# Kernel tuning notes

Measured on AMD Instinct MI355X. Metric: run time of the kernel, lower is better.

Reference implementation:

```python
import jax, jax.numpy as jnp
import numpy as np


def setup_inputs() -> dict:
    key = jax.random.key(0)
    kq, kk, kv = jax.random.split(key, 3)
    B, N, M, H, D = 4, 2048, 2048, 8, 64
    queries = jax.random.normal(kq, (B, N, H, D), dtype=jnp.float32)
    keys = jax.random.normal(kk, (B, M, H, D), dtype=jnp.float32)
    values = jax.random.normal(kv, (B, M, H, D), dtype=jnp.float32)
    return {"queries": queries, "keys": keys, "values": values}


def reference(queries, keys, values):
    # queries: [B,N,H,D], keys/values: [B,M,H,D]
    D = queries.shape[3]
    softmax_temp = 1.0 / (D ** 0.5)
    QK = jnp.einsum('bnhd,bmhd->bnmh', queries, keys)  # [B,N,M,H]
    A = jax.nn.softmax(softmax_temp * QK, axis=2)      # softmax over M
    queried_values = jnp.einsum('bnmh,bmhd->bnhd', A, values)
    attention_weight = jnp.transpose(A, (0, 3, 1, 2))  # [B,H,N,M]
    return (queried_values, attention_weight)
```

## Files before the change

kernel.cpp:

```cpp
#include <hip/hip_runtime.h>

typedef __bf16 bf16x8 __attribute__((ext_vector_type(8)));
typedef float floatx4 __attribute__((ext_vector_type(4)));
typedef unsigned short ushort8 __attribute__((ext_vector_type(8)));
typedef unsigned short ushort4v __attribute__((ext_vector_type(4)));

#define MFMA(a, b, c) __builtin_amdgcn_mfma_f32_16x16x32_bf16((a), (b), (c), 0, 0, 0)

__device__ __forceinline__ unsigned short f2bf(float x) {
  union { float f; unsigned u; } v; v.f = x;
  unsigned r = v.u + 0x7FFFu + ((v.u >> 16) & 1u);
  return (unsigned short)(r >> 16);
}

__global__ __launch_bounds__(256)
void prep(const float* __restrict__ K, const float* __restrict__ V,
          unsigned short* __restrict__ Kb, unsigned short* __restrict__ Vt)
{
  int id = blockIdx.x * 256 + threadIdx.x;
  int isV = id >> 19;
  int cch = id & 524287;
  int bh = cch >> 14;
  int mt = (cch >> 9) & 31;
  int g  = cch & 511;
  int r  = g >> 3;
  int s  = g & 7;
  int e8 = s ^ (r & 7);
  int b = bh >> 3, h = bh & 7;
  ushort8 o;
  if (!isV) {
    const float* p = K + (((size_t)(b * 2048 + mt * 64 + r) * 8 + h) * 64 + e8 * 8);
    float4 x0 = *(const float4*)p;
    float4 x1 = *(const float4*)(p + 4);
    o[0] = f2bf(x0.x); o[1] = f2bf(x0.y); o[2] = f2bf(x0.z); o[3] = f2bf(x0.w);
    o[4] = f2bf(x1.x); o[5] = f2bf(x1.y); o[6] = f2bf(x1.z); o[7] = f2bf(x1.w);
    *(ushort8*)(Kb + (size_t)cch * 8) = o;
  } else {
    const float* p = V + (((size_t)(b * 2048 + mt * 64 + e8 * 8) * 8 + h) * 64 + r);
    #pragma unroll
    for (int j = 0; j < 8; ++j) o[j] = f2bf(p[(size_t)j * 512]);
    *(ushort8*)(Vt + (size_t)cch * 8) = o;
  }
}

__device__ __forceinline__ void stage2k(const unsigned short* gsrc, unsigned short* lds,
                                        int w, int l)
{
  const char* g = (const char*)gsrc + w * 2048 + l * 16;
  char* sd = (char*)lds + w * 2048;
  __builtin_amdgcn_global_load_lds((const __attribute__((address_space(1))) unsigned int*)g,
                                   (__attribute__((address_space(3))) unsigned int*)sd, 16, 0, 0);
  __builtin_amdgcn_global_load_lds((const __attribute__((address_space(1))) unsigned int*)(g + 1024),
                                   (__attribute__((address_space(3))) unsigned int*)(sd + 1024), 16, 0, 0);
}

__device__ __forceinline__ bf16x8 frag(const unsigned short* lds, int r, int bo)
{
  int slot = ((bo >> 4) ^ r) & 7;
  return *(const bf16x8*)((const char*)lds + r * 128 + (slot << 4));
}

__global__ __launch_bounds__(256, 4)
void attn_fwd(const float* __restrict__ Q, const unsigned short* __restrict__ Kb,
              const unsigned short* __restrict__ Vt,
              float* __restrict__ outQV, float* __restrict__ outA)
{
  __shared__ __align__(16) unsigned short Ks[2][4096];
  __shared__ __align__(16) unsigned short Vs[2][4096];
  __shared__ __align__(16) unsigned short As[4096];

  const int tid = threadIdx.x;
  const int w  = tid >> 6;
  const int l  = tid & 63;
  const int c  = l & 15;
  const int q4 = l >> 4;

  const int bx = (blockIdx.x & 7) * 128 + (blockIdx.x >> 3);
  const int qt = bx & 31;
  const int h  = (bx >> 5) & 7;
  const int b  = bx >> 8;
  const int q0 = qt * 64;

  const float scale = 0.125f * 1.44269504088896340736f;

  const size_t base = (size_t)b * (2048 * 512) + (size_t)h * 64;
  const float* Qb = Q + base + (size_t)q0 * 512;

  const unsigned short* Kt0 = Kb + (size_t)(b * 8 + h) * (32 * 4096);
  const unsigned short* Vt0 = Vt + (size_t)(b * 8 + h) * (32 * 4096);

  bf16x8 bQ0, bQ1;
  {
    const float* qp = Qb + (size_t)(16 * w + c) * 512 + q4 * 8;
    float4 qa0 = *(const float4*)(qp);
    float4 qa1 = *(const float4*)(qp + 4);
    float4 qb0 = *(const float4*)(qp + 32);
    float4 qb1 = *(const float4*)(qp + 36);
    ushort8 t0, t1;
    t0[0]=f2bf(qa0.x*scale); t0[1]=f2bf(qa0.y*scale); t0[2]=f2bf(qa0.z*scale); t0[3]=f2bf(qa0.w*scale);
    t0[4]=f2bf(qa1.x*scale); t0[5]=f2bf(qa1.y*scale); t0[6]=f2bf(qa1.z*scale); t0[7]=f2bf(qa1.w*scale);
    t1[0]=f2bf(qb0.x*scale); t1[1]=f2bf(qb0.y*scale); t1[2]=f2bf(qb0.z*scale); t1[3]=f2bf(qb0.w*scale);
    t1[4]=f2bf(qb1.x*scale); t1[5]=f2bf(qb1.y*scale); t1[6]=f2bf(qb1.z*scale); t1[7]=f2bf(qb1.w*scale);
    bQ0 = __builtin_bit_cast(bf16x8, t0);
    bQ1 = __builtin_bit_cast(bf16x8, t1);
  }

  stage2k(Kt0, Ks[0], w, l);
  float lsum[4] = {0.f, 0.f, 0.f, 0.f};
  int cur = 0;
  for (int mt = 0; mt < 32; ++mt) {
    __syncthreads();
    if (mt + 1 < 32) stage2k(Kt0 + (size_t)(mt + 1) * 4096, Ks[cur ^ 1], w, l);
    const unsigned short* Kc = Ks[cur];
    __builtin_amdgcn_s_setprio(1);
    #pragma unroll
    for (int t = 0; t < 4; ++t) {
      bf16x8 aK0 = frag(Kc, t * 16 + c, q4 * 16);
      bf16x8 aK1 = frag(Kc, t * 16 + c, 64 + q4 * 16);
      floatx4 acc = {0.f, 0.f, 0.f, 0.f};
      acc = MFMA(aK0, bQ0, acc);
      acc = MFMA(aK1, bQ1, acc);
      #pragma unroll
      for (int i = 0; i < 4; ++i) lsum[i] += __builtin_amdgcn_exp2f(acc[i]);
    }
    __builtin_amdgcn_s_setprio(0);
    cur ^= 1;
  }
  float rs = (lsum[0] + lsum[1]) + (lsum[2] + lsum[3]);
  rs += __shfl_xor(rs, 16);
  rs += __shfl_xor(rs, 32);
  const float rcp = 1.0f / rs;

  floatx4 Oacc[4];
  #pragma unroll
  for (int t = 0; t < 4; ++t) Oacc[t] = (floatx4){0.f, 0.f, 0.f, 0.f};

  const int arow = 16 * w + c;
  float* aRowP = outA + (((size_t)(b * 8 + h) * 2048 + q0 + arow) * 2048) + q4 * 4;

  __syncthreads();
  stage2k(Kt0, Ks[0], w, l);
  stage2k(Vt0, Vs[0], w, l);
  asm volatile("s_waitcnt vmcnt(0)" ::: "memory");
  __builtin_amdgcn_s_barrier();
  __builtin_amdgcn_sched_barrier(0);
  cur = 0;
  for (int mt = 0; mt < 32; ++mt) {
    if (mt + 1 < 32) {
      stage2k(Kt0 + (size_t)(mt + 1) * 4096, Ks[cur ^ 1], w, l);
      stage2k(Vt0 + (size_t)(mt + 1) * 4096, Vs[cur ^ 1], w, l);
    }
    const unsigned short* Kc = Ks[cur];
    const unsigned short* Vc = Vs[cur];
    const int mc = mt * 64;
    __builtin_amdgcn_s_setprio(1);
    #pragma unroll
    for (int t = 0; t < 4; ++t) {
      bf16x8 aK0 = frag(Kc, t * 16 + c, q4 * 16);
      bf16x8 aK1 = frag(Kc, t * 16 + c, 64 + q4 * 16);
      floatx4 acc = {0.f, 0.f, 0.f, 0.f};
      acc = MFMA(aK0, bQ0, acc);
      acc = MFMA(aK1, bQ1, acc);
      floatx4 av;
      av[0] = __builtin_amdgcn_exp2f(acc[0]) * rcp;
      av[1] = __builtin_amdgcn_exp2f(acc[1]) * rcp;
      av[2] = __builtin_amdgcn_exp2f(acc[2]) * rcp;
      av[3] = __builtin_amdgcn_exp2f(acc[3]) * rcp;
      *(floatx4*)(aRowP + mc + t * 16) = av;
      ushort4v us = { f2bf(av[0]), f2bf(av[1]), f2bf(av[2]), f2bf(av[3]) };
      int bo = t * 32 + q4 * 8;
      int slot = ((bo >> 4) ^ arow) & 7;
      *(ushort4v*)((char*)As + arow * 128 + (slot << 4) + (bo & 15)) = us;
    }
    bf16x8 aP0 = frag(As, arow, q4 * 16);
    bf16x8 aP1 = frag(As, arow, 64 + q4 * 16);
    #pragma unroll
    for (int t = 0; t < 4; ++t) {
      bf16x8 bV0 = frag(Vc, t * 16 + c, q4 * 16);
      bf16x8 bV1 = frag(Vc, t * 16 + c, 64 + q4 * 16);
      Oacc[t] = MFMA(aP0, bV0, Oacc[t]);
      Oacc[t] = MFMA(aP1, bV1, Oacc[t]);
    }
    __builtin_amdgcn_s_setprio(0);
    __builtin_amdgcn_sched_barrier(0);
    asm volatile("s_waitcnt vmcnt(4)" ::: "memory");
    __builtin_amdgcn_s_barrier();
    __builtin_amdgcn_sched_barrier(0);
    cur ^= 1;
  }

  #pragma unroll
  for (int t = 0; t < 4; ++t) {
    #pragma unroll
    for (int i = 0; i < 4; ++i) {
      outQV[base + (size_t)(q0 + 16 * w + q4 * 4 + i) * 512 + t * 16 + c] = Oacc[t][i];
    }
  }
}

extern "C" void kernel_launch(void* const* d_in, const int* in_sizes, int n_in,
                              void* d_out, int out_size, void* d_ws, size_t ws_size,
                              hipStream_t stream)
{
  const float* Q = (const float*)d_in[0];
  const float* K = (const float*)d_in[1];
  const float* V = (const float*)d_in[2];
  float* outQV = (float*)d_out;
  float* outA  = (float*)d_out + 4194304;

  unsigned short* Kb = (unsigned short*)d_ws;
  unsigned short* Vt = (unsigned short*)d_ws + 4194304;

  prep<<<dim3(4096), dim3(256), 0, stream>>>(K, V, Kb, Vt);
  attn_fwd<<<dim3(1024), dim3(256), 0, stream>>>(Q, Kb, Vt, outQV, outA);
}
```

Measured before the change: 634.0 us.

## Double query tile per block and triple-buffer K/V with prefetch distance two

Each block now has 8 waves and covers 128 query rows instead of 64, so every K/V tile staged into LDS serves twice as many queries. Global-to-LDS traffic and block count are halved. K and V staging becomes a three-buffer ring with tiles loaded two iterations ahead, and the waitcnt values are adjusted to match. The cost is more LDS per block (three K/V buffers and a doubled A buffer) and fewer, larger blocks, which may lower occupancy or scheduling flexibility.

```diff
diff --git a/kernel.cpp b/kernel.cpp
--- a/kernel.cpp
+++ b/kernel.cpp
@@ -43,15 +43,13 @@
   }
 }
 
-__device__ __forceinline__ void stage2k(const unsigned short* gsrc, unsigned short* lds,
+__device__ __forceinline__ void stage1k(const unsigned short* gsrc, unsigned short* lds,
                                         int w, int l)
 {
-  const char* g = (const char*)gsrc + w * 2048 + l * 16;
-  char* sd = (char*)lds + w * 2048;
+  const char* g = (const char*)gsrc + w * 1024 + l * 16;
+  char* sd = (char*)lds + w * 1024;
   __builtin_amdgcn_global_load_lds((const __attribute__((address_space(1))) unsigned int*)g,
                                    (__attribute__((address_space(3))) unsigned int*)sd, 16, 0, 0);
-  __builtin_amdgcn_global_load_lds((const __attribute__((address_space(1))) unsigned int*)(g + 1024),
-                                   (__attribute__((address_space(3))) unsigned int*)(sd + 1024), 16, 0, 0);
 }
 
 __device__ __forceinline__ bf16x8 frag(const unsigned short* lds, int r, int bo)
@@ -60,14 +58,14 @@
   return *(const bf16x8*)((const char*)lds + r * 128 + (slot << 4));
 }
 
-__global__ __launch_bounds__(256, 4)
+__global__ __launch_bounds__(512, 4)
 void attn_fwd(const float* __restrict__ Q, const unsigned short* __restrict__ Kb,
               const unsigned short* __restrict__ Vt,
               float* __restrict__ outQV, float* __restrict__ outA)
 {
-  __shared__ __align__(16) unsigned short Ks[2][4096];
-  __shared__ __align__(16) unsigned short Vs[2][4096];
-  __shared__ __align__(16) unsigned short As[4096];
+  __shared__ __align__(16) unsigned short Ks[3][4096];
+  __shared__ __align__(16) unsigned short Vs[3][4096];
+  __shared__ __align__(16) unsigned short As[8192];
 
   const int tid = threadIdx.x;
   const int w  = tid >> 6;
@@ -75,19 +73,20 @@
   const int c  = l & 15;
   const int q4 = l >> 4;
 
-  const int bx = (blockIdx.x & 7) * 128 + (blockIdx.x >> 3);
-  const int qt = bx & 31;
-  const int h  = (bx >> 5) & 7;
-  const int b  = bx >> 8;
-  const int q0 = qt * 64;
+  const int bx = (blockIdx.x & 7) * 64 + (blockIdx.x >> 3);
+  const int qt = bx & 15;
+  const int bh = bx >> 4;
+  const int h  = bh & 7;
+  const int b  = bh >> 3;
+  const int q0 = qt * 128;
 
   const float scale = 0.125f * 1.44269504088896340736f;
 
   const size_t base = (size_t)b * (2048 * 512) + (size_t)h * 64;
   const float* Qb = Q + base + (size_t)q0 * 512;
 
-  const unsigned short* Kt0 = Kb + (size_t)(b * 8 + h) * (32 * 4096);
-  const unsigned short* Vt0 = Vt + (size_t)(b * 8 + h) * (32 * 4096);
+  const unsigned short* Kt0 = Kb + (size_t)bh * (32 * 4096);
+  const unsigned short* Vt0 = Vt + (size_t)bh * (32 * 4096);
 
   bf16x8 bQ0, bQ1;
   {
@@ -105,12 +104,19 @@
     bQ1 = __builtin_bit_cast(bf16x8, t1);
   }
 
-  stage2k(Kt0, Ks[0], w, l);
+  stage1k(Kt0, Ks[0], w, l);
+  stage1k(Kt0 + 4096, Ks[1], w, l);
+  asm volatile("s_waitcnt vmcnt(1)" ::: "memory");
+  __builtin_amdgcn_s_barrier();
+  __builtin_amdgcn_sched_barrier(0);
+
   float lsum[4] = {0.f, 0.f, 0.f, 0.f};
   int cur = 0;
   for (int mt = 0; mt < 32; ++mt) {
-    __syncthreads();
-    if (mt + 1 < 32) stage2k(Kt0 + (size_t)(mt + 1) * 4096, Ks[cur ^ 1], w, l);
+    int nx = (mt + 2 < 32) ? mt + 2 : 31;
+    int sb = cur + 2; if (sb >= 3) sb -= 3;
+    stage1k(Kt0 + (size_t)nx * 4096, Ks[sb], w, l);
+    __builtin_amdgcn_sched_barrier(0);
     const unsigned short* Kc = Ks[cur];
     __builtin_amdgcn_s_setprio(1);
     #pragma unroll
@@ -124,7 +130,11 @@
       for (int i = 0; i < 4; ++i) lsum[i] += __builtin_amdgcn_exp2f(acc[i]);
     }
     __builtin_amdgcn_s_setprio(0);
-    cur ^= 1;
+    __builtin_amdgcn_sched_barrier(0);
+    asm volatile("s_waitcnt vmcnt(1)" ::: "memory");
+    __builtin_amdgcn_s_barrier();
+    __builtin_amdgcn_sched_barrier(0);
+    cur = cur + 1; if (cur >= 3) cur -= 3;
   }
   float rs = (lsum[0] + lsum[1]) + (lsum[2] + lsum[3]);
   rs += __shfl_xor(rs, 16);
@@ -136,20 +146,24 @@
   for (int t = 0; t < 4; ++t) Oacc[t] = (floatx4){0.f, 0.f, 0.f, 0.f};
 
   const int arow = 16 * w + c;
-  float* aRowP = outA + (((size_t)(b * 8 + h) * 2048 + q0 + arow) * 2048) + q4 * 4;
-
-  __syncthreads();
-  stage2k(Kt0, Ks[0], w, l);
-  stage2k(Vt0, Vs[0], w, l);
+  float* aRowP = outA + (((size_t)bh * 2048 + q0 + arow) * 2048) + q4 * 4;
+
   asm volatile("s_waitcnt vmcnt(0)" ::: "memory");
+  stage1k(Kt0, Ks[0], w, l);
+  stage1k(Vt0, Vs[0], w, l);
+  stage1k(Kt0 + 4096, Ks[1], w, l);
+  stage1k(Vt0 + 4096, Vs[1], w, l);
+  asm volatile("s_waitcnt vmcnt(2)" ::: "memory");
   __builtin_amdgcn_s_barrier();
   __builtin_amdgcn_sched_barrier(0);
+
   cur = 0;
   for (int mt = 0; mt < 32; ++mt) {
-    if (mt + 1 < 32) {
-      stage2k(Kt0 + (size_t)(mt + 1) * 4096, Ks[cur ^ 1], w, l);
-      stage2k(Vt0 + (size_t)(mt + 1) * 4096, Vs[cur ^ 1], w, l);
-    }
+    int nx = (mt + 2 < 32) ? mt + 2 : 31;
+    int sb = cur + 2; if (sb >= 3) sb -= 3;
+    stage1k(Kt0 + (size_t)nx * 4096, Ks[sb], w, l);
+    stage1k(Vt0 + (size_t)nx * 4096, Vs[sb], w, l);
+    __builtin_amdgcn_sched_barrier(0);
     const unsigned short* Kc = Ks[cur];
     const unsigned short* Vc = Vs[cur];
     const int mc = mt * 64;
@@ -172,21 +186,25 @@
       int slot = ((bo >> 4) ^ arow) & 7;
       *(ushort4v*)((char*)As + arow * 128 + (slot << 4) + (bo & 15)) = us;
     }
-    bf16x8 aP0 = frag(As, arow, q4 * 16);
-    bf16x8 aP1 = frag(As, arow, 64 + q4 * 16);
-    #pragma unroll
-    for (int t = 0; t < 4; ++t) {
-      bf16x8 bV0 = frag(Vc, t * 16 + c, q4 * 16);
-      bf16x8 bV1 = frag(Vc, t * 16 + c, 64 + q4 * 16);
-      Oacc[t] = MFMA(aP0, bV0, Oacc[t]);
-      Oacc[t] = MFMA(aP1, bV1, Oacc[t]);
+    {
+      int s0 = ((q4) ^ arow) & 7;
+      int s1 = ((4 + q4) ^ arow) & 7;
+      bf16x8 aP0 = *(const bf16x8*)((const char*)As + arow * 128 + (s0 << 4));
+      bf16x8 aP1 = *(const bf16x8*)((const char*)As + arow * 128 + (s1 << 4));
+      #pragma unroll
+      for (int t = 0; t < 4; ++t) {
+        bf16x8 bV0 = frag(Vc, t * 16 + c, q4 * 16);
+        bf16x8 bV1 = frag(Vc, t * 16 + c, 64 + q4 * 16);
+        Oacc[t] = MFMA(aP0, bV0, Oacc[t]);
+        Oacc[t] = MFMA(aP1, bV1, Oacc[t]);
+      }
     }
     __builtin_amdgcn_s_setprio(0);
     __builtin_amdgcn_sched_barrier(0);
-    asm volatile("s_waitcnt vmcnt(4)" ::: "memory");
+    asm volatile("s_waitcnt vmcnt(6)" ::: "memory");
     __builtin_amdgcn_s_barrier();
     __builtin_amdgcn_sched_barrier(0);
-    cur ^= 1;
+    cur = cur + 1; if (cur >= 3) cur -= 3;
   }
 
   #pragma unroll
@@ -212,5 +230,5 @@
   unsigned short* Vt = (unsigned short*)d_ws + 4194304;
 
   prep<<<dim3(4096), dim3(256), 0, stream>>>(K, V, Kb, Vt);
-  attn_fwd<<<dim3(1024), dim3(256), 0, stream>>>(Q, Kb, Vt, outQV, outA);
-}
+  attn_fwd<<<dim3(512), dim3(512), 0, stream>>>(Q, Kb, Vt, outQV, outA);
+}
```

After: 636.1 us. No clear change (+0.3%).
